# Kernel tuning notes

Measured on AMD Instinct MI355X. Metric: run time of the kernel, lower is better.

The kernel has to match this reference:

```python
import jax, jax.numpy as jnp
import numpy as np

N_HEADS = 16


def setup_inputs() -> dict:
    key = jax.random.key(0)
    ks = jax.random.split(key, 5)
    B, S, D = 4, 1024, 1024
    H = N_HEADS
    hs = D // H
    sc = 0.02
    return {
        "x": jax.random.normal(ks[0], (B, S, D), jnp.float32),
        "Wqkv": jax.random.normal(ks[1], (3 * D, D), jnp.float32) * sc,
        "Wout": jax.random.normal(ks[2], (D, D), jnp.float32) * sc,
        "Wpos": jax.random.normal(ks[3], (D, D), jnp.float32) * sc,
        "posn_vect_u": jnp.zeros((1, H, 1, hs), jnp.float32),
        "posn_vect_v": jnp.zeros((1, H, 1, hs), jnp.float32),
        "rel_embed": jax.random.normal(ks[4], (S, D), jnp.float32) * sc,
    }


def reference(x, Wqkv, Wout, Wpos, posn_vect_u, posn_vect_v, rel_embed):
    B, S, D = x.shape
    H = N_HEADS
    hs = D // H

    # qkv projection (torch Linear: y = x @ W.T), split into q,k,v
    qkv = x @ Wqkv.T  # [B,S,3D]
    q, k, v = jnp.split(qkv, 3, axis=-1)
    # [B,S,D] -> [B,H,S,hs]
    q = q.reshape(B, S, H, hs).transpose(0, 2, 1, 3)
    k = k.reshape(B, S, H, hs).transpose(0, 2, 1, 3)
    v = v.reshape(B, S, H, hs).transpose(0, 2, 1, 3)

    # content term: (q + u) @ k^T -> [B,H,S,S]
    attn_dots = jnp.einsum("bhqd,bhkd->bhqk", q + posn_vect_u, k)

    # relative position term (Transformer-XL style)
    rel = rel_embed[-S:] @ Wpos.T          # [S,D]
    rel = rel.T.reshape(H, hs, S)          # [H,hs,S]
    query_posn = jnp.einsum("bhqd,hdk->bhqk", q + posn_vect_v, rel)  # [B,H,S,S]

    # rel-shift gather: shifted[i,j] = query_posn[i, j - i + S - 1]
    i = jnp.arange(S)[:, None]
    j = jnp.arange(S)[None, :]
    idx = jnp.clip(j - i + S - 1, 0, S - 1)  # [S,S]; entries with j>i masked later
    shifted = jnp.take_along_axis(query_posn, idx[None, None], axis=-1)
    attn_dots = attn_dots + shifted

    # causal mask then scaled softmax (matches masked_fill then softmax(x/sqrt(hs)))
    causal = j > i  # [S,S] True above diagonal
    attn_dots = jnp.where(causal[None, None], -jnp.inf, attn_dots)
    scores = jax.nn.softmax(attn_dots / np.sqrt(hs).astype(np.float32), axis=-1)

    attn = jnp.einsum("bhqk,bhkd->bhqd", scores, v)  # [B,H,S,hs]
    out = attn.transpose(0, 2, 1, 3).reshape(B, S, D) @ Wout.T
    return out
```

## Files before the change

### kernel.cpp

```cpp
#include <hip/hip_runtime.h>

#define S_LEN 1024

typedef unsigned short u16;
using bf16x8 = __attribute__((ext_vector_type(8))) short;
using f32x4  = __attribute__((ext_vector_type(4))) float;
using u16x8  = __attribute__((ext_vector_type(8))) unsigned short;
using u16x4  = __attribute__((ext_vector_type(4))) unsigned short;

__device__ __forceinline__ float bf2f(u16 b) {
  unsigned int u = ((unsigned int)b) << 16;
  return __builtin_bit_cast(float, u);
}
__device__ __forceinline__ u16 f2bf(float f) {
  unsigned int u = __builtin_bit_cast(unsigned int, f);
  unsigned int r = u + 0x7fffu + ((u >> 16) & 1u);
  return (u16)(r >> 16);
}

using gas_p = const __attribute__((address_space(1))) void*;
using las_p = __attribute__((address_space(3))) void*;
__device__ __forceinline__ void gload16(const void* g, void* l) {
  __builtin_amdgcn_global_load_lds((gas_p)g, (las_p)l, 16, 0, 0);
}

__global__ __launch_bounds__(256) void cvt_all(const float* __restrict__ x,
    const float* __restrict__ wqkv, const float* __restrict__ wout,
    const float* __restrict__ wpos, const float* __restrict__ rel,
    u16* __restrict__ xb, u16* __restrict__ wqkvb, u16* __restrict__ woutb,
    u16* __restrict__ wposb, u16* __restrict__ relb) {
  int blk = blockIdx.x;
  const float* src; u16* dst; int base;
  if (blk < 4096)      { src = x;    dst = xb;    base = blk; }
  else if (blk < 7168) { src = wqkv; dst = wqkvb; base = blk - 4096; }
  else if (blk < 8192) { src = wout; dst = woutb; base = blk - 7168; }
  else if (blk < 9216) { src = wpos; dst = wposb; base = blk - 8192; }
  else                 { src = rel;  dst = relb;  base = blk - 9216; }
  int i = (base * 256 + threadIdx.x) * 4;
  float4 v = *(const float4*)(src + i);
  u16x4 o;
  o.x = f2bf(v.x); o.y = f2bf(v.y); o.z = f2bf(v.z); o.w = f2bf(v.w);
  *(u16x4*)(dst + i) = o;
}

template <int MODE, int SWZ, int BM64>
__global__ __launch_bounds__(256) void gemm_bt(const u16* __restrict__ A,
    const u16* __restrict__ W, float* __restrict__ Yf, u16* __restrict__ Yb,
    u16* __restrict__ qc, u16* __restrict__ qp,
    const float* __restrict__ uvec, const float* __restrict__ vvec,
    int M, int N, int K) {
  constexpr int BM = BM64 ? 64 : 128;
  constexpr int MI = BM64 ? 2 : 4;
  __shared__ __align__(16) u16 As[2][BM * 32];
  __shared__ __align__(16) u16 Ws[2][128 * 32];
  const int t = threadIdx.x;
  const int w = t >> 6, l = t & 63;
  const int lr = l & 15, lg = l >> 4;
  int bm, bn;
  if (SWZ == 1) {
    int flat = (int)blockIdx.y * 32 + (int)blockIdx.x;
    int xcd = flat & 7, idx = flat >> 3;
    bm = (xcd & 3) * 8 + (idx & 7);
    bn = (xcd >> 2) * 12 + (idx >> 3);
  } else {
    bm = blockIdx.x; bn = blockIdx.y;
  }
  const int wr = BM64 ? ((w >> 1) * 32) : ((w >> 1) * 64);
  const int wc = (w & 1) * 64;
  f32x4 acc[MI][4];
#pragma unroll
  for (int mi = 0; mi < MI; ++mi)
#pragma unroll
    for (int ni = 0; ni < 4; ++ni) acc[mi][ni] = (f32x4){0.f, 0.f, 0.f, 0.f};
  const u16* Ab = A + (size_t)bm * BM * K;
  const u16* Wb = W + (size_t)bn * 128 * K;

  auto stage = [&](int k0, int buf) {
#pragma unroll
    for (int i = 0; i < (BM64 ? 1 : 2); ++i) {
      int c = i * 256 + t;
      gload16(Ab + (size_t)(c >> 2) * K + k0 + (c & 3) * 8, &As[buf][c * 8]);
    }
#pragma unroll
    for (int i = 0; i < 2; ++i) {
      int c = i * 256 + t;
      gload16(Wb + (size_t)(c >> 2) * K + k0 + (c & 3) * 8, &Ws[buf][c * 8]);
    }
  };

  stage(0, 0);
  __syncthreads();
  for (int k0 = 0; k0 < K; k0 += 32) {
    const int cur = (k0 >> 5) & 1;
    if (k0 + 32 < K) stage(k0 + 32, cur ^ 1);
    bf16x8 af[MI], wf[4];
#pragma unroll
    for (int mi = 0; mi < MI; ++mi)
      af[mi] = *(const bf16x8*)&As[cur][(wr + mi * 16 + lr) * 32 + lg * 8];
#pragma unroll
    for (int ni = 0; ni < 4; ++ni)
      wf[ni] = *(const bf16x8*)&Ws[cur][(wc + ni * 16 + lr) * 32 + lg * 8];
    __builtin_amdgcn_s_setprio(1);
#pragma unroll
    for (int mi = 0; mi < MI; ++mi)
#pragma unroll
      for (int ni = 0; ni < 4; ++ni)
        acc[mi][ni] = __builtin_amdgcn_mfma_f32_16x16x32_bf16(af[mi], wf[ni], acc[mi][ni], 0, 0, 0);
    __builtin_amdgcn_s_setprio(0);
    __syncthreads();
  }
#pragma unroll
  for (int mi = 0; mi < MI; ++mi)
#pragma unroll
    for (int ni = 0; ni < 4; ++ni) {
      int col = bn * 128 + wc + ni * 16 + lr;
      if (MODE == 1) {
#pragma unroll
        for (int g = 0; g < 4; ++g) {
          int row = bm * BM + wr + mi * 16 + lg * 4 + g;
          Yf[(size_t)row * N + col] = acc[mi][ni][g];
        }
      } else if (MODE == 0) {
#pragma unroll
        for (int g = 0; g < 4; ++g) {
          int row = bm * BM + wr + mi * 16 + lg * 4 + g;
          Yb[(size_t)row * N + col] = f2bf(acc[mi][ni][g]);
        }
      } else {
        if (col < 1024) {
          float uu = uvec[col], vv = vvec[col];
#pragma unroll
          for (int g = 0; g < 4; ++g) {
            int row = bm * BM + wr + mi * 16 + lg * 4 + g;
            qc[(size_t)row * 1024 + col] = f2bf((acc[mi][ni][g] + uu) * 0.125f);
            qp[(size_t)row * 1024 + col] = f2bf((acc[mi][ni][g] + vv) * 0.125f);
          }
        } else if (col < 2048) {
#pragma unroll
          for (int g = 0; g < 4; ++g) {
            int row = bm * BM + wr + mi * 16 + lg * 4 + g;
            Yb[(size_t)row * 3072 + col] = f2bf(acc[mi][ni][g]);
          }
        } else {
          int row0 = bm * BM + wr + mi * 16 + lg * 4;
          int vrow = (row0 >> 10) * 1024 + (col - 2048);
          u16x4 tmp;
#pragma unroll
          for (int g = 0; g < 4; ++g) tmp[g] = f2bf(acc[mi][ni][g]);
          *(u16x4*)&Yb[(size_t)vrow * 3072 + (row0 & 1023)] = tmp;
        }
      }
    }
}

__global__ __launch_bounds__(256) void attn_fwd(
    const u16* __restrict__ qcb, const u16* __restrict__ qpb,
    const u16* __restrict__ qkv, const u16* __restrict__ relp,
    u16* __restrict__ out) {
  __shared__ __align__(16) u16 Ksb[2][4096];
  __shared__ __align__(16) u16 Vtb[2][4096];
  __shared__ __align__(16) u16 Rs3[3][4096];
  __shared__ __align__(16) float Psf[4][16][68];

  const int flat = (int)blockIdx.y * 8 + (int)blockIdx.x;
  const int wg = (flat & 7) * 64 + (flat >> 3);
  const int sub = wg & 7;
  const int bh = wg >> 3;
  const int b = bh >> 4, h = bh & 15;
  const int t = threadIdx.x;
  const int w = t >> 6, l = t & 63;
  const int lr = l & 15, lg = l >> 4;

  const u16* Kg = qkv + (size_t)b * S_LEN * 3072 + 1024 + h * 64;
  const u16* Vg = qkv + (size_t)bh * 64 * 3072;
  const u16* Rg = relp + h * 64;

  int gl4[4], cg[4];
#pragma unroll
  for (int g = 0; g < 4; ++g) {
    int ql = lg * 4 + g;
    gl4[g] = (l & 48) | ((lr - ql - 1) & 15);
    cg[g] = (lr > ql) ? 1 : 0;
  }

  for (int half = 0; half < 2; ++half) {
    const int qt = half ? sub : (15 - sub);
    const int i0 = qt * 64;
    const int nt = qt + 1;

    bf16x8 qcf[2], qpf[2];
    {
      size_t qoff = (size_t)(b * S_LEN + i0 + w * 16 + lr) * 1024 + h * 64;
      qcf[0] = *(const bf16x8*)(qcb + qoff + lg * 8);
      qcf[1] = *(const bf16x8*)(qcb + qoff + 32 + lg * 8);
      qpf[0] = *(const bf16x8*)(qpb + qoff + lg * 8);
      qpf[1] = *(const bf16x8*)(qpb + qoff + 32 + lg * 8);
    }

    auto stage_k = [&](int j0s, int buf) {
#pragma unroll
      for (int i = 0; i < 2; ++i) {
        int bK = i * 4 + w;
        int ttk = bK >> 1, kc = bK & 1;
        gload16(Kg + (size_t)(j0s + ttk * 16 + lr) * 3072 + kc * 32 + lg * 8,
                &Ksb[buf][bK * 512 + l * 8]);
      }
    };
    auto stage_v = [&](int j0s, int buf) {
#pragma unroll
      for (int i = 0; i < 2; ++i) {
        int bV = i * 4 + w;
        int dt = bV >> 1, kc = bV & 1;
        gload16(Vg + (size_t)(dt * 16 + lr) * 3072 + j0s + kc * 32 + lg * 8,
                &Vtb[buf][bV * 512 + l * 8]);
      }
    };
    auto stage_rchunk = [&](int Gloc, int slot) {
      int Gg = 15 - qt + Gloc;
#pragma unroll
      for (int i = 0; i < 2; ++i) {
        int bR = i * 4 + w;
        int btc = bR >> 1, kc = bR & 1;
        int r = Gg * 64 + btc * 16 + lr;
        r = r > S_LEN - 1 ? S_LEN - 1 : r;
        gload16(Rg + (size_t)r * 1024 + kc * 32 + lg * 8,
                &Rs3[slot][bR * 512 + l * 8]);
      }
    };

    float m_run = -1e30f, l_run = 0.f;
    f32x4 o_acc[4];
#pragma unroll
    for (int dt = 0; dt < 4; ++dt) o_acc[dt] = (f32x4){0.f, 0.f, 0.f, 0.f};

    stage_k(0, 0);
    stage_v(0, 0);
    stage_rchunk(0, 0);
    stage_rchunk(1, 1);
    __syncthreads();

    int sA = 0, sB = 1, sC = 2;
    for (int kt = 0; kt < nt; ++kt) {
      const int cur = kt & 1, nxt = cur ^ 1;
      const int j0 = kt * 64;
      const int have_nxt = (kt + 1 < nt);
      if (have_nxt) {
        stage_k(j0 + 64, nxt);
        stage_v(j0 + 64, nxt);
        stage_rchunk(kt + 2, sC);
      }

      f32x4 sc[4];
      __builtin_amdgcn_s_setprio(1);
#pragma unroll
      for (int tt = 0; tt < 4; ++tt) {
        sc[tt] = (f32x4){0.f, 0.f, 0.f, 0.f};
#pragma unroll
        for (int kc = 0; kc < 2; ++kc) {
          bf16x8 kf = *(const bf16x8*)&Ksb[cur][(tt * 2 + kc) * 512 + l * 8];
          sc[tt] = __builtin_amdgcn_mfma_f32_16x16x32_bf16(qcf[kc], kf, sc[tt], 0, 0, 0);
        }
      }
      f32x4 sp[5];
#pragma unroll
      for (int u5 = 0; u5 < 5; ++u5) {
        int bt = 3 - w + u5;
        const u16* rb = (bt & 4) ? &Rs3[sB][0] : &Rs3[sA][0];
        int btc = bt & 3;
        sp[u5] = (f32x4){0.f, 0.f, 0.f, 0.f};
#pragma unroll
        for (int kc = 0; kc < 2; ++kc) {
          bf16x8 rf = *(const bf16x8*)&rb[(btc * 2 + kc) * 512 + l * 8];
          sp[u5] = __builtin_amdgcn_mfma_f32_16x16x32_bf16(qpf[kc], rf, sp[u5], 0, 0, 0);
        }
      }
      __builtin_amdgcn_s_setprio(0);

#pragma unroll
      for (int g = 0; g < 4; ++g) {
        float bp[5];
#pragma unroll
        for (int u5 = 0; u5 < 5; ++u5) bp[u5] = __shfl(sp[u5][g], gl4[g]);
        int ql = lg * 4 + g;
#pragma unroll
        for (int tt = 0; tt < 4; ++tt) {
          float band = cg[g] ? bp[tt + 1] : bp[tt];
          float z = sc[tt][g] + band;
          if (j0 + tt * 16 + lr > i0 + w * 16 + ql) z = -1e30f;
          Psf[w][ql][tt * 16 + lr] = z;
        }
      }

      float zz[2][8];
#pragma unroll
      for (int kc = 0; kc < 2; ++kc)
#pragma unroll
        for (int h4 = 0; h4 < 2; ++h4) {
          float4 rr = *(const float4*)&Psf[w][lr][kc * 32 + lg * 8 + h4 * 4];
          zz[kc][h4 * 4 + 0] = rr.x; zz[kc][h4 * 4 + 1] = rr.y;
          zz[kc][h4 * 4 + 2] = rr.z; zz[kc][h4 * 4 + 3] = rr.w;
        }
      float mt = zz[0][0];
#pragma unroll
      for (int kc = 0; kc < 2; ++kc)
#pragma unroll
        for (int j = 0; j < 8; ++j) mt = fmaxf(mt, zz[kc][j]);
      mt = fmaxf(mt, __shfl_xor(mt, 16));
      mt = fmaxf(mt, __shfl_xor(mt, 32));
      float mnew = fmaxf(m_run, mt);
      float corr = __expf(m_run - mnew);
      m_run = mnew;
      float s = 0.f;
#pragma unroll
      for (int kc = 0; kc < 2; ++kc)
#pragma unroll
        for (int j = 0; j < 8; ++j) {
          float e = __expf(zz[kc][j] - mnew);
          zz[kc][j] = e;
          s += e;
        }
      s += __shfl_xor(s, 16);
      s += __shfl_xor(s, 32);
      l_run = l_run * corr + s;

      float co[4];
#pragma unroll
      for (int g = 0; g < 4; ++g) co[g] = __shfl(corr, lg * 4 + g);
#pragma unroll
      for (int dt = 0; dt < 4; ++dt)
#pragma unroll
        for (int g = 0; g < 4; ++g) o_acc[dt][g] *= co[g];

      bf16x8 pf[2];
#pragma unroll
      for (int kc = 0; kc < 2; ++kc)
#pragma unroll
        for (int j = 0; j < 8; ++j) pf[kc][j] = (short)f2bf(zz[kc][j]);

      __builtin_amdgcn_s_setprio(1);
#pragma unroll
      for (int dt = 0; dt < 4; ++dt) {
#pragma unroll
        for (int kc = 0; kc < 2; ++kc) {
          bf16x8 vf = *(const bf16x8*)&Vtb[cur][(dt * 2 + kc) * 512 + l * 8];
          o_acc[dt] = __builtin_amdgcn_mfma_f32_16x16x32_bf16(pf[kc], vf, o_acc[dt], 0, 0, 0);
        }
      }
      __builtin_amdgcn_s_setprio(0);
      __syncthreads();
      int stmp = sA; sA = sB; sB = sC; sC = stmp;
    }

    float ll[4];
#pragma unroll
    for (int g = 0; g < 4; ++g) ll[g] = __shfl(l_run, lg * 4 + g);
#pragma unroll
    for (int dt = 0; dt < 4; ++dt) {
      int col = h * 64 + dt * 16 + lr;
#pragma unroll
      for (int g = 0; g < 4; ++g) {
        int row = b * S_LEN + i0 + w * 16 + lg * 4 + g;
        out[(size_t)row * 1024 + col] = f2bf(o_acc[dt][g] / ll[g]);
      }
    }
  }
}

extern "C" void kernel_launch(void* const* d_in, const int* in_sizes, int n_in,
                              void* d_out, int out_size, void* d_ws, size_t ws_size,
                              hipStream_t stream) {
  const float* x    = (const float*)d_in[0];
  const float* Wqkv = (const float*)d_in[1];
  const float* Wout = (const float*)d_in[2];
  const float* Wpos = (const float*)d_in[3];
  const float* u    = (const float*)d_in[4];
  const float* v    = (const float*)d_in[5];
  const float* rel  = (const float*)d_in[6];
  float* out = (float*)d_out;

  u16* ws      = (u16*)d_ws;
  u16* xb      = ws;
  u16* wqkvb   = xb + 4194304;
  u16* woutb   = wqkvb + 3145728;
  u16* wposb   = woutb + 1048576;
  u16* relb    = wposb + 1048576;
  u16* qkvb    = relb + 1048576;
  u16* qcb     = qkvb + 12582912;
  u16* qpb     = qcb + 4194304;
  u16* relproj = qpb + 4194304;
  u16* attno   = relproj + 1048576;

  cvt_all<<<10240, 256, 0, stream>>>(x, Wqkv, Wout, Wpos, rel, xb, wqkvb, woutb, wposb, relb);

  gemm_bt<2, 1, 0><<<dim3(32, 24), 256, 0, stream>>>(xb, wqkvb, nullptr, qkvb, qcb, qpb, u, v, 4096, 3072, 1024);
  gemm_bt<0, 0, 1><<<dim3(16, 8), 256, 0, stream>>>(relb, wposb, nullptr, relproj, nullptr, nullptr, nullptr, nullptr, 1024, 1024, 1024);
  attn_fwd<<<dim3(8, 64), 256, 0, stream>>>(qcb, qpb, qkvb, relproj, attno);
  gemm_bt<1, 0, 1><<<dim3(64, 8), 256, 0, stream>>>(attno, woutb, out, nullptr, nullptr, nullptr, nullptr, nullptr, 4096, 1024, 1024);
}
```

Baseline: 138.6 us.

## Load relative-position tiles directly into registers instead of LDS ring buffer

Removes the three-slot LDS ring buffer for the relative-position projection and instead has each wave load its five banded 16-row R fragments straight from global memory into registers. The load for the next tile is issued right after the positional MFMAs so it overlaps the softmax and PV work. This frees 24 KB of LDS and adds a launch bound of 3 blocks per CU to raise occupancy. In exchange it uses more registers and issues uncoalesced, partly redundant global loads, since waves re-read overlapping rows rather than sharing them through LDS.

```diff
diff --git a/kernel.cpp b/kernel.cpp
--- a/kernel.cpp
+++ b/kernel.cpp
@@ -153,13 +153,12 @@
     }
 }
 
-__global__ __launch_bounds__(256) void attn_fwd(
+__global__ __launch_bounds__(256, 3) void attn_fwd(
     const u16* __restrict__ qcb, const u16* __restrict__ qpb,
     const u16* __restrict__ qkv, const u16* __restrict__ relp,
     u16* __restrict__ out) {
   __shared__ __align__(16) u16 Ksb[2][4096];
   __shared__ __align__(16) u16 Vtb[2][4096];
-  __shared__ __align__(16) u16 Rs3[3][4096];
   __shared__ __align__(16) float Psf[4][16][68];
 
   const int flat = (int)blockIdx.y * 8 + (int)blockIdx.x;
@@ -215,16 +214,16 @@
                 &Vtb[buf][bV * 512 + l * 8]);
       }
     };
-    auto stage_rchunk = [&](int Gloc, int slot) {
-      int Gg = 15 - qt + Gloc;
-#pragma unroll
-      for (int i = 0; i < 2; ++i) {
-        int bR = i * 4 + w;
-        int btc = bR >> 1, kc = bR & 1;
-        int r = Gg * 64 + btc * 16 + lr;
-        r = r > S_LEN - 1 ? S_LEN - 1 : r;
-        gload16(Rg + (size_t)r * 1024 + kc * 32 + lg * 8,
-                &Rs3[slot][bR * 512 + l * 8]);
+    bf16x8 rr[10];
+    auto load_r = [&](int j0s) {
+#pragma unroll
+      for (int u5 = 0; u5 < 5; ++u5) {
+        int bt = 3 - w + u5;
+        int r = j0s - i0 + 960 + bt * 16 + lr;
+        r = r < 0 ? 0 : (r > S_LEN - 1 ? S_LEN - 1 : r);
+#pragma unroll
+        for (int kc = 0; kc < 2; ++kc)
+          rr[u5 * 2 + kc] = *(const bf16x8*)(Rg + (size_t)r * 1024 + kc * 32 + lg * 8);
       }
     };
 
@@ -235,11 +234,9 @@
 
     stage_k(0, 0);
     stage_v(0, 0);
-    stage_rchunk(0, 0);
-    stage_rchunk(1, 1);
+    load_r(0);
     __syncthreads();
 
-    int sA = 0, sB = 1, sC = 2;
     for (int kt = 0; kt < nt; ++kt) {
       const int cur = kt & 1, nxt = cur ^ 1;
       const int j0 = kt * 64;
@@ -247,7 +244,6 @@
       if (have_nxt) {
         stage_k(j0 + 64, nxt);
         stage_v(j0 + 64, nxt);
-        stage_rchunk(kt + 2, sC);
       }
 
       f32x4 sc[4];
@@ -264,17 +260,13 @@
       f32x4 sp[5];
 #pragma unroll
       for (int u5 = 0; u5 < 5; ++u5) {
-        int bt = 3 - w + u5;
-        const u16* rb = (bt & 4) ? &Rs3[sB][0] : &Rs3[sA][0];
-        int btc = bt & 3;
         sp[u5] = (f32x4){0.f, 0.f, 0.f, 0.f};
 #pragma unroll
-        for (int kc = 0; kc < 2; ++kc) {
-          bf16x8 rf = *(const bf16x8*)&rb[(btc * 2 + kc) * 512 + l * 8];
-          sp[u5] = __builtin_amdgcn_mfma_f32_16x16x32_bf16(qpf[kc], rf, sp[u5], 0, 0, 0);
-        }
+        for (int kc = 0; kc < 2; ++kc)
+          sp[u5] = __builtin_amdgcn_mfma_f32_16x16x32_bf16(qpf[kc], rr[u5 * 2 + kc], sp[u5], 0, 0, 0);
       }
       __builtin_amdgcn_s_setprio(0);
+      if (have_nxt) load_r(j0 + 64);
 
 #pragma unroll
       for (int g = 0; g < 4; ++g) {
@@ -296,9 +288,9 @@
       for (int kc = 0; kc < 2; ++kc)
 #pragma unroll
         for (int h4 = 0; h4 < 2; ++h4) {
-          float4 rr = *(const float4*)&Psf[w][lr][kc * 32 + lg * 8 + h4 * 4];
-          zz[kc][h4 * 4 + 0] = rr.x; zz[kc][h4 * 4 + 1] = rr.y;
-          zz[kc][h4 * 4 + 2] = rr.z; zz[kc][h4 * 4 + 3] = rr.w;
+          float4 rv = *(const float4*)&Psf[w][lr][kc * 32 + lg * 8 + h4 * 4];
+          zz[kc][h4 * 4 + 0] = rv.x; zz[kc][h4 * 4 + 1] = rv.y;
+          zz[kc][h4 * 4 + 2] = rv.z; zz[kc][h4 * 4 + 3] = rv.w;
         }
       float mt = zz[0][0];
 #pragma unroll
@@ -348,7 +340,6 @@
       }
       __builtin_amdgcn_s_setprio(0);
       __syncthreads();
-      int stmp = sA; sA = sB; sB = sC; sC = stmp;
     }
 
     float ll[4];
```

Result: slower. 149.9 us (+8.1%).
